# Optimization experiments

Measured on AMD Instinct MI355X. Metric: run time of the kernel, lower is better.

The kernel has to match this reference:

```python
import jax, jax.numpy as jnp
import numpy as np

B, W, LOCAL, GLOBAL = 32, 16, 64, 64
EMB, HIDDEN, OUT, NLAYERS = 256, 512, 64, 3
T = 128  # output_len


def setup_inputs() -> dict:
    key = jax.random.key(0)
    ks = jax.random.split(key, 16)
    s = 0.05
    inp = {
        "z_t": jax.random.normal(ks[0], (B, W, LOCAL), jnp.float32),
        "z_g": jax.random.normal(ks[1], (B, GLOBAL), jnp.float32),
        # embedding: Linear(local+global -> 256, bias=False), torch layout (out,in)
        "w_emb": jax.random.normal(ks[2], (EMB, LOCAL + GLOBAL), jnp.float32) * s,
        # GRU(input_size=1, hidden=256); input is all-zeros so w_ih contributes
        # nothing (only its bias b_ih matters) -> faithfully omit w_ih.
        "gru_w_hh": jax.random.normal(ks[3], (3 * EMB, EMB), jnp.float32) * s,
        "gru_b_ih": jax.random.normal(ks[4], (3 * EMB,), jnp.float32) * s,
        "gru_b_hh": jax.random.normal(ks[5], (3 * EMB,), jnp.float32) * s,
        "mlp_w1": jax.random.normal(ks[6], (HIDDEN, EMB), jnp.float32) * s,
        "mlp_b1": jax.random.normal(ks[7], (HIDDEN,), jnp.float32) * s,
        "mlp_w2": jax.random.normal(ks[8], (HIDDEN, HIDDEN), jnp.float32) * s,
        "mlp_b2": jax.random.normal(ks[9], (HIDDEN,), jnp.float32) * s,
        "mlp_w3": jax.random.normal(ks[10], (HIDDEN, HIDDEN), jnp.float32) * s,
        "mlp_b3": jax.random.normal(ks[11], (HIDDEN,), jnp.float32) * s,
        "mu_w": jax.random.normal(ks[12], (OUT, HIDDEN), jnp.float32) * s,
        "mu_b": jax.random.normal(ks[13], (OUT,), jnp.float32) * s,
        "output_len": T,
    }
    return inp


def _gru_zero_input(h0, w_hh, b_ih, b_hh, length):
    # PyTorch GRU cell with x_t == 0: input-to-hidden term reduces to b_ih.
    b_ir, b_iz, b_in = jnp.split(b_ih, 3)

    def step(h, _):
        gh = h @ w_hh.T + b_hh              # (BW, 3*EMB)
        g_r, g_z, g_n = jnp.split(gh, 3, axis=-1)
        r = jax.nn.sigmoid(b_ir + g_r)
        z = jax.nn.sigmoid(b_iz + g_z)
        n = jnp.tanh(b_in + r * g_n)
        h_new = (1.0 - z) * n + z * h
        return h_new, h_new

    _, hs = jax.lax.scan(step, h0, None, length=length)
    return hs  # (T, BW, EMB)


def reference(z_t, z_g, w_emb, gru_w_hh, gru_b_ih, gru_b_hh,
              mlp_w1, mlp_b1, mlp_w2, mlp_b2, mlp_w3, mlp_b3,
              mu_w, mu_b, output_len):
    b, nw, _ = z_t.shape
    z = jnp.concatenate(
        [z_t, jnp.broadcast_to(z_g[:, None, :], (b, nw, z_g.shape[-1]))], axis=-1)
    emb = z @ w_emb.T                        # (B, W, EMB)
    h0 = emb.reshape(b * nw, -1)             # (BW, EMB) initial hidden state

    hs = _gru_zero_input(h0, gru_w_hh, gru_b_ih, gru_b_hh, output_len)
    h_t = jnp.transpose(hs, (1, 0, 2))       # (BW, T, EMB), batch_first

    # MLP: Linear+ELU (Dropout p=0.05 is identity in eval)
    h = jax.nn.elu(h_t @ mlp_w1.T + mlp_b1)
    h = jax.nn.elu(h @ mlp_w2.T + mlp_b2)
    h = jax.nn.elu(h @ mlp_w3.T + mlp_b3)
    x_mean = h @ mu_w.T + mu_b               # (BW, T, OUT)
    return x_mean.reshape(b, nw * output_len, -1)
```

## Files before the change

### kernel.cpp

```cpp
#include <hip/hip_runtime.h>
#include <hip/hip_bf16.h>


typedef __bf16 bf16_t;
typedef __bf16 bf16x2 __attribute__((ext_vector_type(2)));
typedef __bf16 bf16x4 __attribute__((ext_vector_type(4)));
typedef __bf16 bf16x8 __attribute__((ext_vector_type(8)));
typedef float f32x4 __attribute__((ext_vector_type(4)));

#define MFMA16(a, b, c) __builtin_amdgcn_mfma_f32_16x16x32_bf16(a, b, c, 0, 0, 0)

#define EMB 256
#define TSTEPS 128
#define OUTD 64

#define HS_OFF   0u
#define H0_OFF   33554432u
#define WHH_OFF  34078720u
#define W1_OFF   34471936u
#define W2_OFF   34734080u
#define W3_OFF   35258368u
#define MUW_OFF  35782656u

__device__ __forceinline__ float rcpf(float x){ return __builtin_amdgcn_rcpf(x); }
__device__ __forceinline__ void lds_barrier() {
  asm volatile("s_waitcnt lgkmcnt(0)\n\ts_barrier" ::: "memory");
}
__device__ __forceinline__ float eluf(float x) {
  return (x > 0.f) ? x : (__expf(x) - 1.f);
}
__device__ __forceinline__ bf16x8 cvt8(const float* __restrict__ s) {
  const float4 a = *reinterpret_cast<const float4*>(s);
  const float4 b = *reinterpret_cast<const float4*>(s + 4);
  bf16x8 v;
  v[0] = (bf16_t)a.x; v[1] = (bf16_t)a.y; v[2] = (bf16_t)a.z; v[3] = (bf16_t)a.w;
  v[4] = (bf16_t)b.x; v[5] = (bf16_t)b.y; v[6] = (bf16_t)b.z; v[7] = (bf16_t)b.w;
  return v;
}

template<int KC, int LOGKC>
__device__ __forceinline__ void conv_frag8(
    const float* __restrict__ src, bf16_t* __restrict__ dst,
    int NK8, int g, int G)
{
  const int K = KC * 128;
  for (int i8 = g; i8 < NK8; i8 += G) {
    const int l15  = i8 & 15;
    const int quad = (i8 >> 4) & 3;
    const int kk   = (i8 >> 6) & 3;
    const int rem  = i8 >> 8;
    const int kc   = rem & (KC - 1);
    const int nt   = rem >> LOGKC;
    *reinterpret_cast<bf16x8*>(dst + (size_t)i8 * 8) =
        cvt8(src + (size_t)(nt * 16 + l15) * K + kc * 128 + kk * 32 + quad * 8);
  }
}

__global__ __launch_bounds__(256) void ce_kernel(
    const float* __restrict__ z_t, const float* __restrict__ z_g,
    const float* __restrict__ w_emb, float* __restrict__ h0,
    const float* __restrict__ whh, const float* __restrict__ w1,
    const float* __restrict__ w2, const float* __restrict__ w3,
    const float* __restrict__ muw, char* __restrict__ ws)
{
  const int tid = threadIdx.x;
  if (blockIdx.x < 512) {
    __shared__ float zrow[128];
    const int bw = blockIdx.x;
    if (tid < 128)
      zrow[tid] = (tid < 64) ? z_t[bw * 64 + tid] : z_g[(bw >> 4) * 64 + (tid - 64)];
    __syncthreads();
    const float4* wp = reinterpret_cast<const float4*>(w_emb + (size_t)tid * 128);
    float s = 0.f;
#pragma unroll
    for (int k4 = 0; k4 < 32; ++k4) {
      const float4 w = wp[k4];
      s += zrow[k4 * 4 + 0] * w.x + zrow[k4 * 4 + 1] * w.y
         + zrow[k4 * 4 + 2] * w.z + zrow[k4 * 4 + 3] * w.w;
    }
    h0[(size_t)bw * 256 + tid] = s;
  } else {
    const int g = (blockIdx.x - 512) * 256 + tid;
    const int G = 256 * 256;
    bf16_t* d = (bf16_t*)(ws + WHH_OFF);
    for (int i8 = g; i8 < 24576; i8 += G)
      *reinterpret_cast<bf16x8*>(d + (size_t)i8 * 8) = cvt8(whh + (size_t)i8 * 8);
    conv_frag8<2, 1>(w1,  (bf16_t*)(ws + W1_OFF),  16384, g, G);
    conv_frag8<4, 2>(w2,  (bf16_t*)(ws + W2_OFF),  32768, g, G);
    conv_frag8<4, 2>(w3,  (bf16_t*)(ws + W3_OFF),  32768, g, G);
    conv_frag8<4, 2>(muw, (bf16_t*)(ws + MUW_OFF),  4096, g, G);
  }
}

__global__ __launch_bounds__(512, 2) void gru_kernel(
    const float* __restrict__ h0, const bf16_t* __restrict__ w_hh,
    const float* __restrict__ b_ih, const float* __restrict__ b_hh,
    bf16_t* __restrict__ hs)
{
  __shared__ __align__(16) bf16_t h16[2][16][272];

  const int tid  = threadIdx.x;
  const int wv   = tid >> 6;
  const int lane = tid & 63;
  const int l15  = lane & 15;
  const int quad = lane >> 4;
  const int bw0  = blockIdx.x * 4;
  const int cA   = wv * 32 + l15;

  bf16x8 wf[6][8];
#pragma unroll
  for (int g = 0; g < 3; ++g)
#pragma unroll
    for (int s = 0; s < 2; ++s) {
      const int n = g * 256 + cA + s * 16;
#pragma unroll
      for (int kk = 0; kk < 8; ++kk)
        wf[g * 2 + s][kk] = *reinterpret_cast<const bf16x8*>(
            w_hh + (size_t)n * 256 + kk * 32 + quad * 8);
    }

  float br[2], bz[2], bin[2], bhn[2], hm[2];
#pragma unroll
  for (int s = 0; s < 2; ++s) {
    const int c = cA + s * 16;
    br[s]  = b_ih[c]       + b_hh[c];
    bz[s]  = b_ih[256 + c] + b_hh[256 + c];
    bin[s] = b_ih[512 + c];
    bhn[s] = b_hh[512 + c];
    hm[s]  = h0[(size_t)(bw0 + quad) * 256 + c];
  }

  {
    bf16x8 zv;
#pragma unroll
    for (int e = 0; e < 8; ++e) zv[e] = (bf16_t)0.f;
    for (int i = tid; i < 1088; i += 512)
      reinterpret_cast<bf16x8*>(h16)[i] = zv;
  }
  __syncthreads();
#pragma unroll
  for (int s = 0; s < 2; ++s)
    h16[0][quad * 4][cA + s * 16] = (bf16_t)hm[s];
  __syncthreads();

  bf16_t* hsp = hs + ((size_t)(bw0 + quad) * TSTEPS) * EMB + cA;

#pragma unroll 1
  for (int t = 0; t < TSTEPS; ++t) {
    const bf16_t (*hr)[272] = h16[t & 1];
    bf16_t (*hw)[272] = h16[(t & 1) ^ 1];

    f32x4 acc[6] = {};
#pragma unroll
    for (int kk = 0; kk < 8; ++kk) {
      const bf16x8 a = *reinterpret_cast<const bf16x8*>(&hr[l15][kk * 32 + quad * 8]);
#pragma unroll
      for (int ct = 0; ct < 6; ++ct)
        acc[ct] = MFMA16(a, wf[ct][kk], acc[ct]);
    }

#pragma unroll
    for (int s = 0; s < 2; ++s) {
      const float gr = acc[s][0]     + br[s];
      const float gz = acc[2 + s][0] + bz[s];
      const float gn = acc[4 + s][0] + bhn[s];
      const float rr = rcpf(1.f + __expf(-gr));
      const float zz = rcpf(1.f + __expf(-gz));
      const float pre = bin[s] + rr * gn;
      const float nn = 1.f - 2.f * rcpf(__expf(2.f * pre) + 1.f);
      hm[s] = nn + zz * (hm[s] - nn);
      const bf16_t nh = (bf16_t)hm[s];
      hw[quad * 4][cA + s * 16] = nh;
      hsp[(size_t)t * EMB + s * 16] = nh;
    }
    lds_barrier();
  }
}

template<int KC>
__device__ __forceinline__ void mlp_layer(
    const bf16_t* __restrict__ Wf, const float* __restrict__ bias,
    bf16_t (*act)[536], int wv, int lane, int l15, int quad)
{
  constexpr int NIT = KC * 4;
  f32x4 acc[4][8] = {};
  bf16x8 wf[2][4];

#pragma unroll
  for (int ct = 0; ct < 4; ++ct)
    wf[0][ct] = *reinterpret_cast<const bf16x8*>(
        Wf + (((size_t)(wv * 4 + ct) * KC) << 11) + lane * 8);

#pragma unroll
  for (int it = 0; it < NIT; ++it) {
    const int cur = it & 1, nxt = cur ^ 1;
    if (it + 1 < NIT) {
      const int kc1 = (it + 1) >> 2, kk1 = (it + 1) & 3;
#pragma unroll
      for (int ct = 0; ct < 4; ++ct)
        wf[nxt][ct] = *reinterpret_cast<const bf16x8*>(
            Wf + ((((size_t)(wv * 4 + ct) * KC + kc1) * 4 + kk1) << 9) + lane * 8);
    }
    const int kc = it >> 2, kk = it & 3;
    bf16x8 a8[8];
#pragma unroll
    for (int mt = 0; mt < 8; ++mt)
      a8[mt] = *reinterpret_cast<const bf16x8*>(
          &act[mt * 16 + l15][kc * 128 + kk * 32 + quad * 8]);
#pragma unroll
    for (int mt = 0; mt < 8; ++mt)
#pragma unroll
      for (int ct = 0; ct < 4; ++ct)
        acc[ct][mt] = MFMA16(wf[cur][ct], a8[mt], acc[ct][mt]);
  }

  __syncthreads();
#pragma unroll
  for (int ct = 0; ct < 4; ++ct) {
    const int nb = (wv * 4 + ct) * 16 + quad * 4;
    const float4 b4 = *reinterpret_cast<const float4*>(bias + nb);
#pragma unroll
    for (int mt = 0; mt < 8; ++mt) {
      bf16x4 v;
      v[0] = (bf16_t)eluf(acc[ct][mt][0] + b4.x);
      v[1] = (bf16_t)eluf(acc[ct][mt][1] + b4.y);
      v[2] = (bf16_t)eluf(acc[ct][mt][2] + b4.z);
      v[3] = (bf16_t)eluf(acc[ct][mt][3] + b4.w);
      *reinterpret_cast<bf16x4*>(&act[mt * 16 + l15][nb]) = v;
    }
  }
  __syncthreads();
}

__global__ __launch_bounds__(512, 2) void mlp_kernel(
    const bf16_t* __restrict__ hs,
    const bf16_t* __restrict__ w1, const float* __restrict__ b1,
    const bf16_t* __restrict__ w2, const float* __restrict__ b2,
    const bf16_t* __restrict__ w3, const float* __restrict__ b3,
    const bf16_t* __restrict__ muw, const float* __restrict__ mub,
    float* __restrict__ out)
{
  __shared__ __align__(16) bf16_t act[128][536];

  const int tid  = threadIdx.x;
  const int wv   = tid >> 6;
  const int lane = tid & 63;
  const int l15  = lane & 15;
  const int quad = lane >> 4;
  const size_t r0 = (size_t)blockIdx.x * 128;

  for (int v = tid; v < 128 * 32; v += 512) {
    const int rr = v >> 5, cc = v & 31;
    bf16x8 x = *reinterpret_cast<const bf16x8*>(hs + (r0 + rr) * EMB + cc * 8);
    *reinterpret_cast<bf16x8*>(&act[rr][cc * 8]) = x;
  }
  __syncthreads();

  mlp_layer<2>(w1, b1, act, wv, lane, l15, quad);
  mlp_layer<4>(w2, b2, act, wv, lane, l15, quad);
  mlp_layer<4>(w3, b3, act, wv, lane, l15, quad);

  f32x4 macc[4] = {};
  const int nt  = wv & 3;
  const int n   = nt * 16 + l15;
  const int mtb = (wv >> 2) * 4;
#pragma unroll
  for (int it = 0; it < 16; ++it) {
    const int kc = it >> 2, kk = it & 3;
    bf16x8 wfm = *reinterpret_cast<const bf16x8*>(
        muw + ((((size_t)nt * 4 + kc) * 4 + kk) << 9) + lane * 8);
#pragma unroll
    for (int i = 0; i < 4; ++i) {
      bf16x8 a = *reinterpret_cast<const bf16x8*>(
          &act[(mtb + i) * 16 + l15][kc * 128 + kk * 32 + quad * 8]);
      macc[i] = MFMA16(a, wfm, macc[i]);
    }
  }
  const float mb = mub[n];
#pragma unroll
  for (int i = 0; i < 4; ++i)
#pragma unroll
    for (int r = 0; r < 4; ++r)
      out[(r0 + (mtb + i) * 16 + quad * 4 + r) * OUTD + n] = macc[i][r] + mb;
}

extern "C" void kernel_launch(void* const* d_in, const int* in_sizes, int n_in,
                              void* d_out, int out_size, void* d_ws, size_t ws_size,
                              hipStream_t stream) {
  char* ws = (char*)d_ws;

  ce_kernel<<<768, 256, 0, stream>>>(
      (const float*)d_in[0], (const float*)d_in[1], (const float*)d_in[2],
      (float*)(ws + H0_OFF),
      (const float*)d_in[3], (const float*)d_in[6], (const float*)d_in[8],
      (const float*)d_in[10], (const float*)d_in[12], ws);

  gru_kernel<<<128, 512, 0, stream>>>(
      (const float*)(ws + H0_OFF), (const bf16_t*)(ws + WHH_OFF),
      (const float*)d_in[4], (const float*)d_in[5],
      (bf16_t*)(ws + HS_OFF));

  mlp_kernel<<<512, 512, 0, stream>>>(
      (const bf16_t*)(ws + HS_OFF),
      (const bf16_t*)(ws + W1_OFF), (const float*)d_in[7],
      (const bf16_t*)(ws + W2_OFF), (const float*)d_in[9],
      (const bf16_t*)(ws + W3_OFF), (const float*)d_in[11],
      (const bf16_t*)(ws + MUW_OFF), (const float*)d_in[13],
      (float*)d_out);
}
```

Baseline: 313.9 us.

## Split MLP kernel work across 16 waves with 2D row/column wave tiling

The MLP kernel goes from 512 to 1024 threads per block. Each wave now owns a 4x4 tile of 16x16 output blocks, indexed by column group and row group, where it previously owned a 4x8 strip over all rows. The double-buffered weight prefetch is dropped, so weights are loaded each iteration without overlap. The intent is to cut per-wave accumulator registers and add latency hiding through more waves per block. The cost is weight loads repeated by two row groups and the loss of explicit load/compute overlap.

```diff
diff --git a/kernel.cpp b/kernel.cpp
--- a/kernel.cpp
+++ b/kernel.cpp
@@ -180,59 +180,50 @@
 template<int KC>
 __device__ __forceinline__ void mlp_layer(
     const bf16_t* __restrict__ Wf, const float* __restrict__ bias,
-    bf16_t (*act)[536], int wv, int lane, int l15, int quad)
+    bf16_t (*act)[536], int cg, int rg, int lane, int l15, int quad)
 {
   constexpr int NIT = KC * 4;
-  f32x4 acc[4][8] = {};
-  bf16x8 wf[2][4];
-
-#pragma unroll
-  for (int ct = 0; ct < 4; ++ct)
-    wf[0][ct] = *reinterpret_cast<const bf16x8*>(
-        Wf + (((size_t)(wv * 4 + ct) * KC) << 11) + lane * 8);
+  f32x4 acc[4][4] = {};
 
 #pragma unroll
   for (int it = 0; it < NIT; ++it) {
-    const int cur = it & 1, nxt = cur ^ 1;
-    if (it + 1 < NIT) {
-      const int kc1 = (it + 1) >> 2, kk1 = (it + 1) & 3;
+    const int kc = it >> 2, kk = it & 3;
+    bf16x8 wf[4];
+#pragma unroll
+    for (int ct = 0; ct < 4; ++ct)
+      wf[ct] = *reinterpret_cast<const bf16x8*>(
+          Wf + ((((size_t)(cg * 4 + ct) * KC + kc) * 4 + kk) << 9) + lane * 8);
+    bf16x8 a8[4];
+#pragma unroll
+    for (int mt = 0; mt < 4; ++mt)
+      a8[mt] = *reinterpret_cast<const bf16x8*>(
+          &act[(rg * 4 + mt) * 16 + l15][kc * 128 + kk * 32 + quad * 8]);
+#pragma unroll
+    for (int mt = 0; mt < 4; ++mt)
 #pragma unroll
       for (int ct = 0; ct < 4; ++ct)
-        wf[nxt][ct] = *reinterpret_cast<const bf16x8*>(
-            Wf + ((((size_t)(wv * 4 + ct) * KC + kc1) * 4 + kk1) << 9) + lane * 8);
-    }
-    const int kc = it >> 2, kk = it & 3;
-    bf16x8 a8[8];
-#pragma unroll
-    for (int mt = 0; mt < 8; ++mt)
-      a8[mt] = *reinterpret_cast<const bf16x8*>(
-          &act[mt * 16 + l15][kc * 128 + kk * 32 + quad * 8]);
-#pragma unroll
-    for (int mt = 0; mt < 8; ++mt)
-#pragma unroll
-      for (int ct = 0; ct < 4; ++ct)
-        acc[ct][mt] = MFMA16(wf[cur][ct], a8[mt], acc[ct][mt]);
+        acc[ct][mt] = MFMA16(wf[ct], a8[mt], acc[ct][mt]);
   }
 
   __syncthreads();
 #pragma unroll
   for (int ct = 0; ct < 4; ++ct) {
-    const int nb = (wv * 4 + ct) * 16 + quad * 4;
+    const int nb = (cg * 4 + ct) * 16 + quad * 4;
     const float4 b4 = *reinterpret_cast<const float4*>(bias + nb);
 #pragma unroll
-    for (int mt = 0; mt < 8; ++mt) {
+    for (int mt = 0; mt < 4; ++mt) {
       bf16x4 v;
       v[0] = (bf16_t)eluf(acc[ct][mt][0] + b4.x);
       v[1] = (bf16_t)eluf(acc[ct][mt][1] + b4.y);
       v[2] = (bf16_t)eluf(acc[ct][mt][2] + b4.z);
       v[3] = (bf16_t)eluf(acc[ct][mt][3] + b4.w);
-      *reinterpret_cast<bf16x4*>(&act[mt * 16 + l15][nb]) = v;
-    }
-  }
-  __syncthreads();
-}
-
-__global__ __launch_bounds__(512, 2) void mlp_kernel(
+      *reinterpret_cast<bf16x4*>(&act[(rg * 4 + mt) * 16 + l15][nb]) = v;
+    }
+  }
+  __syncthreads();
+}
+
+__global__ __launch_bounds__(1024) void mlp_kernel(
     const bf16_t* __restrict__ hs,
     const bf16_t* __restrict__ w1, const float* __restrict__ b1,
     const bf16_t* __restrict__ w2, const float* __restrict__ b2,
@@ -243,34 +234,36 @@
   __shared__ __align__(16) bf16_t act[128][536];
 
   const int tid  = threadIdx.x;
-  const int wv   = tid >> 6;
+  const int w    = tid >> 6;
   const int lane = tid & 63;
   const int l15  = lane & 15;
   const int quad = lane >> 4;
+  const int cg   = w & 7;
+  const int rg   = w >> 3;
   const size_t r0 = (size_t)blockIdx.x * 128;
 
-  for (int v = tid; v < 128 * 32; v += 512) {
+  for (int v = tid; v < 128 * 32; v += 1024) {
     const int rr = v >> 5, cc = v & 31;
     bf16x8 x = *reinterpret_cast<const bf16x8*>(hs + (r0 + rr) * EMB + cc * 8);
     *reinterpret_cast<bf16x8*>(&act[rr][cc * 8]) = x;
   }
   __syncthreads();
 
-  mlp_layer<2>(w1, b1, act, wv, lane, l15, quad);
-  mlp_layer<4>(w2, b2, act, wv, lane, l15, quad);
-  mlp_layer<4>(w3, b3, act, wv, lane, l15, quad);
-
-  f32x4 macc[4] = {};
-  const int nt  = wv & 3;
+  mlp_layer<2>(w1, b1, act, cg, rg, lane, l15, quad);
+  mlp_layer<4>(w2, b2, act, cg, rg, lane, l15, quad);
+  mlp_layer<4>(w3, b3, act, cg, rg, lane, l15, quad);
+
+  f32x4 macc[2] = {};
+  const int nt  = w & 3;
   const int n   = nt * 16 + l15;
-  const int mtb = (wv >> 2) * 4;
+  const int mtb = (w >> 2) * 2;
 #pragma unroll
   for (int it = 0; it < 16; ++it) {
     const int kc = it >> 2, kk = it & 3;
     bf16x8 wfm = *reinterpret_cast<const bf16x8*>(
         muw + ((((size_t)nt * 4 + kc) * 4 + kk) << 9) + lane * 8);
 #pragma unroll
-    for (int i = 0; i < 4; ++i) {
+    for (int i = 0; i < 2; ++i) {
       bf16x8 a = *reinterpret_cast<const bf16x8*>(
           &act[(mtb + i) * 16 + l15][kc * 128 + kk * 32 + quad * 8]);
       macc[i] = MFMA16(a, wfm, macc[i]);
@@ -278,7 +271,7 @@
   }
   const float mb = mub[n];
 #pragma unroll
-  for (int i = 0; i < 4; ++i)
+  for (int i = 0; i < 2; ++i)
 #pragma unroll
     for (int r = 0; r < 4; ++r)
       out[(r0 + (mtb + i) * 16 + quad * 4 + r) * OUTD + n] = macc[i][r] + mb;
@@ -300,7 +293,7 @@
       (const float*)d_in[4], (const float*)d_in[5],
       (bf16_t*)(ws + HS_OFF));
 
-  mlp_kernel<<<512, 512, 0, stream>>>(
+  mlp_kernel<<<512, 1024, 0, stream>>>(
       (const bf16_t*)(ws + HS_OFF),
       (const bf16_t*)(ws + W1_OFF), (const float*)d_in[7],
       (const bf16_t*)(ws + W2_OFF), (const float*)d_in[9],
```

Result: slower. 359.1 us (+14.4%).
